# Performance work log

Measured on AMD Instinct MI355X. Metric: run time of the kernel, lower is better.

## Reference

```python
import itertools, math
import jax, jax.numpy as jnp
import numpy as np

N_QUBITS = 8
N_LAYERS = 2
D = 2 ** N_QUBITS
B = 16384
PAIRS = list(itertools.combinations(range(N_QUBITS), 2))
N_PAIRS = len(PAIRS)


def _static():
    s = np.arange(D)
    # ising_masks[p, s] = +1 if bits qi,qj of s differ else -1
    masks = np.stack([
        np.where((((s >> (N_QUBITS - 1 - qi)) & 1) ^ ((s >> (N_QUBITS - 1 - qj)) & 1)).astype(bool), 1.0, -1.0).astype(np.float32)
        for qi, qj in PAIRS])
    # z_signs[k, s] = +1 if bit k of s is 0 else -1
    zsig = np.stack([
        np.where(((s >> (N_QUBITS - 1 - k)) & 1).astype(bool), -1.0, 1.0).astype(np.float32)
        for k in range(N_QUBITS)])
    # CNOT is a permutation: src[i] = i ^ target_mask if ctrl bit of i set, else i
    cidx = np.empty((N_LAYERS, N_QUBITS, D), np.int32)
    for l in range(N_LAYERS):
        rng = l % (N_QUBITS - 1) + 1 if N_QUBITS > 1 else 1
        for ctrl in range(N_QUBITS):
            tgt = (ctrl + rng) % N_QUBITS
            bit = ((s >> (N_QUBITS - 1 - ctrl)) & 1).astype(bool)
            cidx[l, ctrl] = np.where(bit, s ^ (1 << (N_QUBITS - 1 - tgt)), s)
    return jnp.asarray(masks), jnp.asarray(zsig), jnp.asarray(cidx)

ISING_MASKS, Z_SIGNS, CNOT_IDX = _static()


def _ry(a):
    # a: [...] -> [..., 2, 2] complex64
    c, sn = jnp.cos(a * 0.5), jnp.sin(a * 0.5)
    return jnp.stack([jnp.stack([c, -sn], -1), jnp.stack([sn, c], -1)], -2).astype(jnp.complex64)


def _rz(a):
    h = a.astype(jnp.complex64) * 0.5
    z = jnp.zeros_like(h)
    return jnp.stack([jnp.stack([jnp.exp(-1j * h), z], -1), jnp.stack([z, jnp.exp(1j * h)], -1)], -2)


def _rot(w):
    # w: [3] = (phi, theta, omega) -> Rot = RZ(omega) @ RY(theta) @ RZ(phi), shape [2,2]
    return _rz(w[2]) @ _ry(w[1]) @ _rz(w[0])


def _apply_1q(state, gate, k):
    # state: [B, D]; gate: [B,2,2] (batched) or [2,2] (shared)
    Bs, Ds = state.shape
    hi, lo = 1 << k, 1 << (N_QUBITS - k - 1)
    s = state.reshape(Bs, hi, 2, lo)
    if gate.ndim == 3:
        s = jnp.einsum('bij,bhjl->bhil', gate, s)
    else:
        s = jnp.einsum('ij,bhjl->bhil', gate, s)
    return s.reshape(Bs, Ds)


def _forward(theta, phi_enc, j_upper, vqc_weights):
    Bs = theta.shape[0]
    state = jnp.zeros((Bs, D), jnp.complex64).at[:, 0].set(1.0)
    # encoding layer
    for k in range(N_QUBITS):
        state = _apply_1q(state, _ry(theta[:, k]), k)
        state = _apply_1q(state, _rz(phi_enc[:, k]), k)
    # IsingZZ: product over pairs of exp(0.5j*pi*J_p*mask_p) == exp of sum
    exponent = (0.5 * math.pi) * (j_upper @ ISING_MASKS)  # [B, D], real
    state = state * jnp.exp(1j * exponent.astype(jnp.complex64))
    for l in range(N_LAYERS):
        for k in range(N_QUBITS):
            state = _apply_1q(state, _rot(vqc_weights[l, k]), k)
        for k in range(N_QUBITS):
            # CNOT ring as gather permutation (same math as state @ cnot.mT)
            state = jnp.take(state, CNOT_IDX[l, k], axis=1)
        if l < N_LAYERS - 1:
            for k in range(N_QUBITS):
                state = _apply_1q(state, _ry(theta[:, k] * 0.5), k)
                state = _apply_1q(state, _rz(phi_enc[:, k] * 0.5), k)
    probs = jnp.abs(state) ** 2  # [B, D] float32
    return (probs @ Z_SIGNS.T).astype(theta.dtype)  # [B, N_QUBITS]


def setup_inputs() -> dict:
    key = jax.random.key(0)
    k1, k2, k3, k4 = jax.random.split(key, 4)
    return {
        'theta': jax.random.normal(k1, (B, N_QUBITS), jnp.float32),
        'phi_enc': jax.random.normal(k2, (B, N_QUBITS), jnp.float32),
        'j_upper': jax.random.normal(k3, (B, N_PAIRS), jnp.float32),
        'vqc_weights': jax.random.normal(k4, (N_LAYERS, N_QUBITS, 3), jnp.float32),
    }


def reference(theta, phi_enc, j_upper, vqc_weights):
    return _forward(theta, phi_enc, j_upper, vqc_weights)
```

## Files before the change

### kernel.cpp

```cpp
#include <hip/hip_runtime.h>


using f2 = __attribute__((ext_vector_type(2))) float;

__device__ __forceinline__ f2 cmul2(f2 w, f2 z) {
    f2 r;
    r.x = w.x * z.x - w.y * z.y;
    r.y = w.x * z.y + w.y * z.x;
    return r;
}
__device__ __forceinline__ f2 cmadd(f2 acc, f2 w, f2 z) {
    acc.x += w.x * z.x - w.y * z.y;
    acc.y += w.x * z.y + w.y * z.x;
    return acc;
}

__device__ __forceinline__ f2 shflx(f2 v, int m) {
    f2 r; r.x = __shfl_xor(v.x, m, 64); r.y = __shfl_xor(v.y, m, 64); return r;
}

__device__ __forceinline__ float uxor(float f, unsigned u) {
    return __uint_as_float(__float_as_uint(f) ^ u);
}

__device__ __forceinline__ f2 enc_sel(float t, float p, bool hi) {
    float s_, c_, sp_, cp_;
    __sincosf(t * 0.5f, &s_, &c_);
    __sincosf(p * 0.5f, &sp_, &cp_);
    const float m = hi ? s_ : c_;
    f2 r; r.x = m * cp_; r.y = hi ? m * sp_ : -m * sp_;
    return r;
}

template<int VREG, int VLANE, int UREG>
__device__ __forceinline__ void gateU(f2 (&s)[16],
                                      float g00r, float giP, float brP, float g01i)
{
    if constexpr (VLANE == 0) {
        constexpr int pivot = VREG & (-VREG);
        #pragma unroll
        for (int j = 0; j < 16; ++j) {
            if ((j & pivot) != 0) continue;
            const int j2 = j ^ VREG;
            const f2 x = s[j], y = s[j2];
            {
                const bool n = (__builtin_popcount(j & UREG) & 1) != 0;
                const float gi = n ? -giP : giP, br = n ? -brP : brP;
                s[j].x = fmaf(-g01i, y.y, fmaf(br, y.x, fmaf(-gi, x.y, g00r * x.x)));
                s[j].y = fmaf( g01i, y.x, fmaf(br, y.y, fmaf( gi, x.x, g00r * x.y)));
            }
            {
                const bool n = (__builtin_popcount(j2 & UREG) & 1) != 0;
                const float gi = n ? -giP : giP, br = n ? -brP : brP;
                s[j2].x = fmaf(-g01i, x.y, fmaf(br, x.x, fmaf(-gi, y.y, g00r * y.x)));
                s[j2].y = fmaf( g01i, x.x, fmaf(br, x.y, fmaf( gi, y.x, g00r * y.y)));
            }
        }
    } else if constexpr (VREG == 0) {
        #pragma unroll
        for (int j = 0; j < 16; ++j) {
            const f2 w = shflx(s[j], VLANE);
            const f2 x = s[j];
            const bool n = (__builtin_popcount(j & UREG) & 1) != 0;
            const float gi = n ? -giP : giP, br = n ? -brP : brP;
            s[j].x = fmaf(-g01i, w.y, fmaf(br, w.x, fmaf(-gi, x.y, g00r * x.x)));
            s[j].y = fmaf( g01i, w.x, fmaf(br, w.y, fmaf( gi, x.x, g00r * x.y)));
        }
    } else {
        constexpr int pivot = VREG & (-VREG);
        #pragma unroll
        for (int j = 0; j < 16; ++j) {
            if ((j & pivot) != 0) continue;
            const int j2 = j ^ VREG;
            const f2 p1 = shflx(s[j2], VLANE);
            const f2 p2 = shflx(s[j],  VLANE);
            const f2 x = s[j], y = s[j2];
            {
                const bool n = (__builtin_popcount(j & UREG) & 1) != 0;
                const float gi = n ? -giP : giP, br = n ? -brP : brP;
                s[j].x = fmaf(-g01i, p1.y, fmaf(br, p1.x, fmaf(-gi, x.y, g00r * x.x)));
                s[j].y = fmaf( g01i, p1.x, fmaf(br, p1.y, fmaf( gi, x.x, g00r * x.y)));
            }
            {
                const bool n = (__builtin_popcount(j2 & UREG) & 1) != 0;
                const float gi = n ? -giP : giP, br = n ? -brP : brP;
                s[j2].x = fmaf(-g01i, p2.y, fmaf(br, p2.x, fmaf(-gi, y.y, g00r * y.x)));
                s[j2].y = fmaf( g01i, p2.x, fmaf(br, p2.y, fmaf( gi, y.x, g00r * y.y)));
            }
        }
    }
}

#define ROT0(K, VR, VL, UR, SL) do {                                    \
    const float4 g_ = *reinterpret_cast<const float4*>(gates + (K)*4);  \
    gateU<VR, VL, UR>(s, g_.x, uxor(g_.y, SL), uxor(g_.z, SL), g_.w);   \
} while (0)

#define FUSED(K, VR, VL, UR, SL) do {                                   \
    const float4 g_ = *reinterpret_cast<const float4*>(gates + (8+(K))*4); \
    const f2 R00 = {g_.x, g_.y}, R01 = {g_.z, g_.w};                    \
    float c_, s_, cp_, sp_;                                             \
    __sincosf(th[K] * 0.25f, &s_, &c_);                                 \
    __sincosf(ph[K] * 0.25f, &sp_, &cp_);                               \
    const f2 E00 = { c_*cp_, -c_*sp_}, E10 = { s_*cp_,  s_*sp_};        \
    const f2 E01 = {-s_*cp_,  s_*sp_}, E11 = { c_*cp_,  c_*sp_};        \
    const f2 F00 = cmadd(cmul2(R00, E00), R01, E10);                    \
    const f2 F01 = cmadd(cmul2(R00, E01), R01, E11);                    \
    gateU<VR, VL, UR>(s, F00.x, uxor(F00.y, SL), uxor(F01.x, SL), F01.y); \
} while (0)

__global__ __launch_bounds__(64) void prep_gates(const float* __restrict__ w,
                                                 float* __restrict__ g)
{
    const int t = threadIdx.x;
    if (t < 16) {
        const float wph = w[t*3+0], wth = w[t*3+1], wom = w[t*3+2];
        float c_, s_, ca_, sa_, cb_, sb_;
        __sincosf(wth * 0.5f, &s_, &c_);
        __sincosf(0.5f * (wph + wom), &sa_, &ca_);
        __sincosf(0.5f * (wph - wom), &sb_, &cb_);
        float* o = g + t * 4;
        o[0] =  c_*ca_;  o[1] = -c_*sa_;
        o[2] = -s_*cb_;  o[3] = -s_*sb_;
    }
}

__global__ __launch_bounds__(64, 4) void vqc_kernel(
    const float* __restrict__ theta,
    const float* __restrict__ phi,
    const float* __restrict__ jup,
    const float* __restrict__ gates,
    float* __restrict__ out,
    int Btot)
{
    const int wid    = blockIdx.x;
    const int lane   = threadIdx.x & 63;
    const int lane16 = lane & 15;
    const int bq     = wid * 4 + (lane >> 4);
    const int b      = bq < Btot ? bq : Btot - 1;

    float th[8], ph[8];
    {
        const float4* t4 = reinterpret_cast<const float4*>(theta + (size_t)b * 8);
        const float4* p4 = reinterpret_cast<const float4*>(phi   + (size_t)b * 8);
        const float4 a = t4[0], c = t4[1], d = p4[0], e = p4[1];
        th[0]=a.x; th[1]=a.y; th[2]=a.z; th[3]=a.w;
        th[4]=c.x; th[5]=c.y; th[6]=c.z; th[7]=c.w;
        ph[0]=d.x; ph[1]=d.y; ph[2]=d.z; ph[3]=d.w;
        ph[4]=e.x; ph[5]=e.y; ph[6]=e.z; ph[7]=e.w;
    }

    const unsigned s8 = (unsigned)(lane16 & 8) << 28;
    const unsigned s4 = (unsigned)(lane16 & 4) << 29;
    const unsigned s2 = (unsigned)(lane16 & 2) << 30;
    const unsigned s1 = (unsigned)(lane16 & 1) << 31;
    const unsigned sC = s8 ^ s4;
    const unsigned sE = sC ^ s2;
    const unsigned sF = sE ^ s1;

    f2 P = enc_sel(th[4], ph[4], (lane16 & 8) != 0);
    P = cmul2(P, enc_sel(th[5], ph[5], (lane16 & 4) != 0));
    P = cmul2(P, enc_sel(th[6], ph[6], (lane16 & 2) != 0));
    P = cmul2(P, enc_sel(th[7], ph[7], (lane16 & 1) != 0));

    f2 m01[4], m23[4];
    {
        float s0, c0, sp0, cp0, s1_, c1_, sp1, cp1;
        __sincosf(th[0]*0.5f, &s0, &c0); __sincosf(ph[0]*0.5f, &sp0, &cp0);
        __sincosf(th[1]*0.5f, &s1_, &c1_); __sincosf(ph[1]*0.5f, &sp1, &cp1);
        const f2 A0={c0*cp0,-c0*sp0}, A1={s0*cp0,s0*sp0};
        const f2 B0={c1_*cp1,-c1_*sp1}, B1={s1_*cp1,s1_*sp1};
        #pragma unroll
        for (int a = 0; a < 4; ++a)
            m01[a] = cmul2((a & 2) ? A1 : A0, (a & 1) ? B1 : B0);
        __sincosf(th[2]*0.5f, &s0, &c0); __sincosf(ph[2]*0.5f, &sp0, &cp0);
        __sincosf(th[3]*0.5f, &s1_, &c1_); __sincosf(ph[3]*0.5f, &sp1, &cp1);
        const f2 C0={c0*cp0,-c0*sp0}, C1={s0*cp0,s0*sp0};
        const f2 D0={c1_*cp1,-c1_*sp1}, D1={s1_*cp1,s1_*sp1};
        #pragma unroll
        for (int a = 0; a < 4; ++a)
            m23[a] = cmul2((a & 2) ? C1 : C0, (a & 1) ? D1 : D0);
    }

    float c01, c02, c03, c12, c13, c23, Q0, Q1, Q2, Q3, LL;
    {
        const float4* J4 = reinterpret_cast<const float4*>(jup + (size_t)b * 28);
        const float z4 = (lane16 & 8) ? -1.f : 1.f;
        const float z5 = (lane16 & 4) ? -1.f : 1.f;
        const float z6 = (lane16 & 2) ? -1.f : 1.f;
        const float z7 = (lane16 & 1) ? -1.f : 1.f;
        const float4 x0 = J4[0], x1 = J4[1], x2 = J4[2], x3 = J4[3];
        const float4 x4 = J4[4], x5 = J4[5], x6 = J4[6];
        c01 = x0.x; c02 = x0.y; c03 = x0.z;
        Q0  = x0.w*z4 + x1.x*z5 + x1.y*z6 + x1.z*z7;
        c12 = x1.w; c13 = x2.x;
        Q1  = x2.y*z4 + x2.z*z5 + x2.w*z6 + x3.x*z7;
        c23 = x3.y;
        Q2  = x3.z*z4 + x3.w*z5 + x4.x*z6 + x4.y*z7;
        Q3  = x4.z*z4 + x4.w*z5 + x5.x*z6 + x5.y*z7;
        LL  = x5.z*(z4*z5) + x5.w*(z4*z6) + x6.x*(z4*z7)
            + x6.y*(z5*z6) + x6.z*(z5*z7) + x6.w*(z6*z7);
    }

    f2 s[16];
    constexpr float HPI = 1.5707963267948966f;
    #pragma unroll
    for (int j = 0; j < 16; ++j) {
        f2 u = cmul2(cmul2(m01[j >> 2], m23[j & 3]), P);
        float S = LL;
        S += ((__builtin_popcount(j & 0xC) & 1) ? -c01 : c01);
        S += ((__builtin_popcount(j & 0xA) & 1) ? -c02 : c02);
        S += ((__builtin_popcount(j & 0x9) & 1) ? -c03 : c03);
        S += ((__builtin_popcount(j & 0x6) & 1) ? -c12 : c12);
        S += ((__builtin_popcount(j & 0x5) & 1) ? -c13 : c13);
        S += ((__builtin_popcount(j & 0x3) & 1) ? -c23 : c23);
        S += ((j & 8) ? -Q0 : Q0);
        S += ((j & 4) ? -Q1 : Q1);
        S += ((j & 2) ? -Q2 : Q2);
        S += ((j & 1) ? -Q3 : Q3);
        float se, ce;
        __sincosf(-HPI * S, &se, &ce);
        s[j] = cmul2(u, (f2){ce, se});
    }

    ROT0(0, 0x8, 0x0, 0x8, 0u);
    ROT0(1, 0x4, 0x0, 0x4, 0u);
    ROT0(2, 0x2, 0x0, 0x2, 0u);
    ROT0(3, 0x1, 0x0, 0x1, 0u);
    ROT0(4, 0x0, 0x8, 0x0, s8);
    ROT0(5, 0x0, 0x4, 0x0, s4);
    ROT0(6, 0x0, 0x2, 0x0, s2);
    ROT0(7, 0x0, 0x1, 0x0, s1);

    FUSED(0, 0xC, 0x0, 0x7, sF);
    FUSED(1, 0x6, 0x0, 0xC, 0u);
    FUSED(2, 0x3, 0x0, 0xE, 0u);
    FUSED(3, 0x1, 0x8, 0xF, 0u);
    FUSED(4, 0x0, 0xC, 0xF, s8);
    FUSED(5, 0x0, 0x6, 0xF, sC);
    FUSED(6, 0x0, 0x3, 0xF, sE);
    FUSED(7, 0xC, 0x1, 0xF, sF);

    float p[16];
    #pragma unroll
    for (int j = 0; j < 16; ++j) p[j] = fmaf(s[j].y, s[j].y, s[j].x * s[j].x);
    #pragma unroll
    for (int st = 1; st < 16; st <<= 1) {
        #pragma unroll
        for (int j = 0; j < 16; ++j) {
            if ((j & st) != 0) continue;
            const float a = p[j], bb = p[j | st];
            p[j] = a + bb;  p[j | st] = a - bb;
        }
    }
    float o[8];
    o[0] = (__popc(lane16 & 0x6) & 1) ? -p[0xE] : p[0xE];
    o[1] = (__popc(lane16 & 0x3) & 1) ? -p[0xF] : p[0xF];
    o[2] = (__popc(lane16 & 0xF) & 1) ? -p[0x9] : p[0x9];
    o[3] = p[0x3];
    o[4] = (__popc(lane16 & 0x7) & 1) ? -p[0x6] : p[0x6];
    o[5] = (__popc(lane16 & 0xC) & 1) ? -p[0xC] : p[0xC];
    o[6] = (__popc(lane16 & 0x9) & 1) ? -p[0x9] : p[0x9];
    o[7] = (__popc(lane16 & 0x3) & 1) ? -p[0x3] : p[0x3];

    #pragma unroll
    for (int m = 1; m <= 8; m <<= 1) {
        #pragma unroll
        for (int q = 0; q < 8; ++q) o[q] += __shfl_xor(o[q], m, 64);
    }

    if (lane16 == 0 && bq < Btot) {
        float4* op = reinterpret_cast<float4*>(out + (size_t)bq * 8);
        op[0] = make_float4(o[0], o[1], o[2], o[3]);
        op[1] = make_float4(o[4], o[5], o[6], o[7]);
    }
}

extern "C" void kernel_launch(void* const* d_in, const int* in_sizes, int n_in,
                              void* d_out, int out_size, void* d_ws, size_t ws_size,
                              hipStream_t stream) {
    const float* theta = (const float*)d_in[0];
    const float* phi   = (const float*)d_in[1];
    const float* jup   = (const float*)d_in[2];
    const float* w     = (const float*)d_in[3];
    float* out   = (float*)d_out;
    float* gates = (float*)d_ws;

    const int B = in_sizes[0] / 8;
    hipLaunchKernelGGL(prep_gates, dim3(1), dim3(64), 0, stream, w, gates);

    const int blocks = (B + 3) / 4;
    hipLaunchKernelGGL(vqc_kernel, dim3(blocks), dim3(64), 0, stream,
                       theta, phi, jup, gates, out, B);
}
```

Measured before the change: 82.54 us.

## Spread each sample over 32 lanes and fold gate prep into main kernel

Each 256-qubit state is now split across 32 lanes holding 8 amplitudes each, instead of 16 lanes holding 16, so the per-thread register footprint shrinks and more lanes work on each sample. The separate prep_gates launch is removed. Each lane now computes the rotation gate matrices itself and shares them through readlane, and the fused encoding-rotation gates are precomputed per lane and broadcast with shuffles. The trade-off is more cross-lane shuffles per gate, one extra reduction stage, and redundant trig work in every wave.

```diff
diff --git a/kernel.cpp b/kernel.cpp
--- a/kernel.cpp
+++ b/kernel.cpp
@@ -33,13 +33,13 @@
 }
 
 template<int VREG, int VLANE, int UREG>
-__device__ __forceinline__ void gateU(f2 (&s)[16],
-                                      float g00r, float giP, float brP, float g01i)
+__device__ __forceinline__ void gateU8(f2 (&s)[8],
+                                       float g00r, float giP, float brP, float g01i)
 {
     if constexpr (VLANE == 0) {
         constexpr int pivot = VREG & (-VREG);
         #pragma unroll
-        for (int j = 0; j < 16; ++j) {
+        for (int j = 0; j < 8; ++j) {
             if ((j & pivot) != 0) continue;
             const int j2 = j ^ VREG;
             const f2 x = s[j], y = s[j2];
@@ -58,7 +58,7 @@
         }
     } else if constexpr (VREG == 0) {
         #pragma unroll
-        for (int j = 0; j < 16; ++j) {
+        for (int j = 0; j < 8; ++j) {
             const f2 w = shflx(s[j], VLANE);
             const f2 x = s[j];
             const bool n = (__builtin_popcount(j & UREG) & 1) != 0;
@@ -69,7 +69,7 @@
     } else {
         constexpr int pivot = VREG & (-VREG);
         #pragma unroll
-        for (int j = 0; j < 16; ++j) {
+        for (int j = 0; j < 8; ++j) {
             if ((j & pivot) != 0) continue;
             const int j2 = j ^ VREG;
             const f2 p1 = shflx(s[j2], VLANE);
@@ -91,53 +91,45 @@
     }
 }
 
-#define ROT0(K, VR, VL, UR, SL) do {                                    \
-    const float4 g_ = *reinterpret_cast<const float4*>(gates + (K)*4);  \
-    gateU<VR, VL, UR>(s, g_.x, uxor(g_.y, SL), uxor(g_.z, SL), g_.w);   \
+#define RL(x, t) __int_as_float(__builtin_amdgcn_readlane(__float_as_int(x), (t)))
+
+#define ROT0(K, VR, VL, UR, SL) do {                                       \
+    const float g0r = RL(q00r, K), g0i = RL(q00i, K);                      \
+    const float g1r = RL(q01r, K), g1i = RL(q01i, K);                      \
+    gateU8<VR, VL, UR>(s, g0r, uxor(g0i, SL), uxor(g1r, SL), g1i);         \
 } while (0)
 
-#define FUSED(K, VR, VL, UR, SL) do {                                   \
-    const float4 g_ = *reinterpret_cast<const float4*>(gates + (8+(K))*4); \
-    const f2 R00 = {g_.x, g_.y}, R01 = {g_.z, g_.w};                    \
-    float c_, s_, cp_, sp_;                                             \
-    __sincosf(th[K] * 0.25f, &s_, &c_);                                 \
-    __sincosf(ph[K] * 0.25f, &sp_, &cp_);                               \
-    const f2 E00 = { c_*cp_, -c_*sp_}, E10 = { s_*cp_,  s_*sp_};        \
-    const f2 E01 = {-s_*cp_,  s_*sp_}, E11 = { c_*cp_,  c_*sp_};        \
-    const f2 F00 = cmadd(cmul2(R00, E00), R01, E10);                    \
-    const f2 F01 = cmadd(cmul2(R00, E01), R01, E11);                    \
-    gateU<VR, VL, UR>(s, F00.x, uxor(F00.y, SL), uxor(F01.x, SL), F01.y); \
+#define FUSED(K, VR, VL, UR, SL) do {                                      \
+    const float f0r = __shfl(F00x, K, 8), f0i = __shfl(F00y, K, 8);        \
+    const float f1r = __shfl(F01x, K, 8), f1i = __shfl(F01y, K, 8);        \
+    gateU8<VR, VL, UR>(s, f0r, uxor(f0i, SL), uxor(f1r, SL), f1i);         \
 } while (0)
 
-__global__ __launch_bounds__(64) void prep_gates(const float* __restrict__ w,
-                                                 float* __restrict__ g)
-{
-    const int t = threadIdx.x;
-    if (t < 16) {
-        const float wph = w[t*3+0], wth = w[t*3+1], wom = w[t*3+2];
-        float c_, s_, ca_, sa_, cb_, sb_;
-        __sincosf(wth * 0.5f, &s_, &c_);
-        __sincosf(0.5f * (wph + wom), &sa_, &ca_);
-        __sincosf(0.5f * (wph - wom), &sb_, &cb_);
-        float* o = g + t * 4;
-        o[0] =  c_*ca_;  o[1] = -c_*sa_;
-        o[2] = -s_*cb_;  o[3] = -s_*sb_;
-    }
-}
-
-__global__ __launch_bounds__(64, 4) void vqc_kernel(
+__global__ __launch_bounds__(256, 7) void vqc_kernel(
     const float* __restrict__ theta,
     const float* __restrict__ phi,
     const float* __restrict__ jup,
-    const float* __restrict__ gates,
+    const float* __restrict__ w,
     float* __restrict__ out,
     int Btot)
 {
-    const int wid    = blockIdx.x;
-    const int lane   = threadIdx.x & 63;
-    const int lane16 = lane & 15;
-    const int bq     = wid * 4 + (lane >> 4);
-    const int b      = bq < Btot ? bq : Btot - 1;
+    const int gtid  = blockIdx.x * 256 + threadIdx.x;
+    const int lane  = threadIdx.x & 63;
+    const int lane5 = lane & 31;
+    const int bq    = gtid >> 5;
+    const int b     = bq < Btot ? bq : Btot - 1;
+
+    float q00r, q00i, q01r, q01i;
+    {
+        const int gt = lane & 15;
+        const float wph = w[gt*3+0], wth = w[gt*3+1], wom = w[gt*3+2];
+        float gc_, gs_, ca_, sa_, cb_, sb_;
+        __sincosf(wth * 0.5f, &gs_, &gc_);
+        __sincosf(0.5f * (wph + wom), &sa_, &ca_);
+        __sincosf(0.5f * (wph - wom), &sb_, &cb_);
+        q00r =  gc_*ca_;  q00i = -gc_*sa_;
+        q01r = -gs_*cb_;  q01i = -gs_*sb_;
+    }
 
     float th[8], ph[8];
     {
@@ -150,126 +142,137 @@
         ph[4]=e.x; ph[5]=e.y; ph[6]=e.z; ph[7]=e.w;
     }
 
-    const unsigned s8 = (unsigned)(lane16 & 8) << 28;
-    const unsigned s4 = (unsigned)(lane16 & 4) << 29;
-    const unsigned s2 = (unsigned)(lane16 & 2) << 30;
-    const unsigned s1 = (unsigned)(lane16 & 1) << 31;
-    const unsigned sC = s8 ^ s4;
-    const unsigned sE = sC ^ s2;
-    const unsigned sF = sE ^ s1;
-
-    f2 P = enc_sel(th[4], ph[4], (lane16 & 8) != 0);
-    P = cmul2(P, enc_sel(th[5], ph[5], (lane16 & 4) != 0));
-    P = cmul2(P, enc_sel(th[6], ph[6], (lane16 & 2) != 0));
-    P = cmul2(P, enc_sel(th[7], ph[7], (lane16 & 1) != 0));
-
-    f2 m01[4], m23[4];
-    {
-        float s0, c0, sp0, cp0, s1_, c1_, sp1, cp1;
+    float F00x, F00y, F01x, F01y;
+    {
+        const int Kq = lane5 & 7;
+        const float thK = theta[(size_t)b * 8 + Kq];
+        const float phK = phi  [(size_t)b * 8 + Kq];
+        float c_, s_, cp_, sp_;
+        __sincosf(thK * 0.25f, &s_, &c_);
+        __sincosf(phK * 0.25f, &sp_, &cp_);
+        const f2 R00 = { __shfl(q00r, 8 + Kq, 16), __shfl(q00i, 8 + Kq, 16) };
+        const f2 R01 = { __shfl(q01r, 8 + Kq, 16), __shfl(q01i, 8 + Kq, 16) };
+        const f2 E00 = { c_*cp_, -c_*sp_}, E10 = { s_*cp_,  s_*sp_};
+        const f2 E01 = {-s_*cp_,  s_*sp_}, E11 = { c_*cp_,  c_*sp_};
+        const f2 F00 = cmadd(cmul2(R00, E00), R01, E10);
+        const f2 F01 = cmadd(cmul2(R00, E01), R01, E11);
+        F00x = F00.x; F00y = F00.y; F01x = F01.x; F01y = F01.y;
+    }
+
+    const unsigned t16 = (unsigned)(lane5 & 16) << 27;
+    const unsigned t8  = (unsigned)(lane5 & 8)  << 28;
+    const unsigned t4  = (unsigned)(lane5 & 4)  << 29;
+    const unsigned t2  = (unsigned)(lane5 & 2)  << 30;
+    const unsigned t1  = (unsigned)(lane5 & 1)  << 31;
+    const unsigned s18 = t16 ^ t8;
+    const unsigned s1C = s18 ^ t4;
+    const unsigned s1E = s1C ^ t2;
+    const unsigned s1F = s1E ^ t1;
+
+    f2 P = enc_sel(th[3], ph[3], (lane5 & 16) != 0);
+    P = cmul2(P, enc_sel(th[4], ph[4], (lane5 & 8) != 0));
+    P = cmul2(P, enc_sel(th[5], ph[5], (lane5 & 4) != 0));
+    P = cmul2(P, enc_sel(th[6], ph[6], (lane5 & 2) != 0));
+    P = cmul2(P, enc_sel(th[7], ph[7], (lane5 & 1) != 0));
+
+    f2 m012[8];
+    {
+        float s0, c0, sp0, cp0;
         __sincosf(th[0]*0.5f, &s0, &c0); __sincosf(ph[0]*0.5f, &sp0, &cp0);
-        __sincosf(th[1]*0.5f, &s1_, &c1_); __sincosf(ph[1]*0.5f, &sp1, &cp1);
         const f2 A0={c0*cp0,-c0*sp0}, A1={s0*cp0,s0*sp0};
-        const f2 B0={c1_*cp1,-c1_*sp1}, B1={s1_*cp1,s1_*sp1};
-        #pragma unroll
-        for (int a = 0; a < 4; ++a)
-            m01[a] = cmul2((a & 2) ? A1 : A0, (a & 1) ? B1 : B0);
+        __sincosf(th[1]*0.5f, &s0, &c0); __sincosf(ph[1]*0.5f, &sp0, &cp0);
+        const f2 B0={c0*cp0,-c0*sp0}, B1={s0*cp0,s0*sp0};
         __sincosf(th[2]*0.5f, &s0, &c0); __sincosf(ph[2]*0.5f, &sp0, &cp0);
-        __sincosf(th[3]*0.5f, &s1_, &c1_); __sincosf(ph[3]*0.5f, &sp1, &cp1);
         const f2 C0={c0*cp0,-c0*sp0}, C1={s0*cp0,s0*sp0};
-        const f2 D0={c1_*cp1,-c1_*sp1}, D1={s1_*cp1,s1_*sp1};
-        #pragma unroll
-        for (int a = 0; a < 4; ++a)
-            m23[a] = cmul2((a & 2) ? C1 : C0, (a & 1) ? D1 : D0);
-    }
-
-    float c01, c02, c03, c12, c13, c23, Q0, Q1, Q2, Q3, LL;
+        #pragma unroll
+        for (int a = 0; a < 8; ++a)
+            m012[a] = cmul2(cmul2((a & 4) ? A1 : A0, (a & 2) ? B1 : B0),
+                            (a & 1) ? C1 : C0);
+    }
+
+    float c01, c02, c12, Q0, Q1, Q2, LL;
     {
         const float4* J4 = reinterpret_cast<const float4*>(jup + (size_t)b * 28);
-        const float z4 = (lane16 & 8) ? -1.f : 1.f;
-        const float z5 = (lane16 & 4) ? -1.f : 1.f;
-        const float z6 = (lane16 & 2) ? -1.f : 1.f;
-        const float z7 = (lane16 & 1) ? -1.f : 1.f;
+        const float z3 = (lane5 & 16) ? -1.f : 1.f;
+        const float z4 = (lane5 & 8)  ? -1.f : 1.f;
+        const float z5 = (lane5 & 4)  ? -1.f : 1.f;
+        const float z6 = (lane5 & 2)  ? -1.f : 1.f;
+        const float z7 = (lane5 & 1)  ? -1.f : 1.f;
         const float4 x0 = J4[0], x1 = J4[1], x2 = J4[2], x3 = J4[3];
         const float4 x4 = J4[4], x5 = J4[5], x6 = J4[6];
-        c01 = x0.x; c02 = x0.y; c03 = x0.z;
-        Q0  = x0.w*z4 + x1.x*z5 + x1.y*z6 + x1.z*z7;
-        c12 = x1.w; c13 = x2.x;
-        Q1  = x2.y*z4 + x2.z*z5 + x2.w*z6 + x3.x*z7;
-        c23 = x3.y;
-        Q2  = x3.z*z4 + x3.w*z5 + x4.x*z6 + x4.y*z7;
-        Q3  = x4.z*z4 + x4.w*z5 + x5.x*z6 + x5.y*z7;
-        LL  = x5.z*(z4*z5) + x5.w*(z4*z6) + x6.x*(z4*z7)
+        c01 = x0.x; c02 = x0.y; c12 = x1.w;
+        Q0  = x0.z*z3 + x0.w*z4 + x1.x*z5 + x1.y*z6 + x1.z*z7;
+        Q1  = x2.x*z3 + x2.y*z4 + x2.z*z5 + x2.w*z6 + x3.x*z7;
+        Q2  = x3.y*z3 + x3.z*z4 + x3.w*z5 + x4.x*z6 + x4.y*z7;
+        LL  = x4.z*(z3*z4) + x4.w*(z3*z5) + x5.x*(z3*z6) + x5.y*(z3*z7)
+            + x5.z*(z4*z5) + x5.w*(z4*z6) + x6.x*(z4*z7)
             + x6.y*(z5*z6) + x6.z*(z5*z7) + x6.w*(z6*z7);
     }
 
-    f2 s[16];
+    f2 s[8];
     constexpr float HPI = 1.5707963267948966f;
     #pragma unroll
-    for (int j = 0; j < 16; ++j) {
-        f2 u = cmul2(cmul2(m01[j >> 2], m23[j & 3]), P);
+    for (int j = 0; j < 8; ++j) {
+        f2 u = cmul2(m012[j], P);
         float S = LL;
-        S += ((__builtin_popcount(j & 0xC) & 1) ? -c01 : c01);
-        S += ((__builtin_popcount(j & 0xA) & 1) ? -c02 : c02);
-        S += ((__builtin_popcount(j & 0x9) & 1) ? -c03 : c03);
-        S += ((__builtin_popcount(j & 0x6) & 1) ? -c12 : c12);
-        S += ((__builtin_popcount(j & 0x5) & 1) ? -c13 : c13);
-        S += ((__builtin_popcount(j & 0x3) & 1) ? -c23 : c23);
-        S += ((j & 8) ? -Q0 : Q0);
-        S += ((j & 4) ? -Q1 : Q1);
-        S += ((j & 2) ? -Q2 : Q2);
-        S += ((j & 1) ? -Q3 : Q3);
+        S += ((__builtin_popcount(j & 6) & 1) ? -c01 : c01);
+        S += ((__builtin_popcount(j & 5) & 1) ? -c02 : c02);
+        S += ((__builtin_popcount(j & 3) & 1) ? -c12 : c12);
+        S += ((j & 4) ? -Q0 : Q0);
+        S += ((j & 2) ? -Q1 : Q1);
+        S += ((j & 1) ? -Q2 : Q2);
         float se, ce;
         __sincosf(-HPI * S, &se, &ce);
         s[j] = cmul2(u, (f2){ce, se});
     }
 
-    ROT0(0, 0x8, 0x0, 0x8, 0u);
-    ROT0(1, 0x4, 0x0, 0x4, 0u);
-    ROT0(2, 0x2, 0x0, 0x2, 0u);
-    ROT0(3, 0x1, 0x0, 0x1, 0u);
-    ROT0(4, 0x0, 0x8, 0x0, s8);
-    ROT0(5, 0x0, 0x4, 0x0, s4);
-    ROT0(6, 0x0, 0x2, 0x0, s2);
-    ROT0(7, 0x0, 0x1, 0x0, s1);
-
-    FUSED(0, 0xC, 0x0, 0x7, sF);
-    FUSED(1, 0x6, 0x0, 0xC, 0u);
-    FUSED(2, 0x3, 0x0, 0xE, 0u);
-    FUSED(3, 0x1, 0x8, 0xF, 0u);
-    FUSED(4, 0x0, 0xC, 0xF, s8);
-    FUSED(5, 0x0, 0x6, 0xF, sC);
-    FUSED(6, 0x0, 0x3, 0xF, sE);
-    FUSED(7, 0xC, 0x1, 0xF, sF);
-
-    float p[16];
-    #pragma unroll
-    for (int j = 0; j < 16; ++j) p[j] = fmaf(s[j].y, s[j].y, s[j].x * s[j].x);
-    #pragma unroll
-    for (int st = 1; st < 16; st <<= 1) {
-        #pragma unroll
-        for (int j = 0; j < 16; ++j) {
+    ROT0(0, 0x4, 0x00, 0x4, 0u);
+    ROT0(1, 0x2, 0x00, 0x2, 0u);
+    ROT0(2, 0x1, 0x00, 0x1, 0u);
+    ROT0(3, 0x0, 0x10, 0x0, t16);
+    ROT0(4, 0x0, 0x08, 0x0, t8);
+    ROT0(5, 0x0, 0x04, 0x0, t4);
+    ROT0(6, 0x0, 0x02, 0x0, t2);
+    ROT0(7, 0x0, 0x01, 0x0, t1);
+
+    FUSED(0, 0x6, 0x00, 0x3, s1F);
+    FUSED(1, 0x3, 0x00, 0x6, 0u);
+    FUSED(2, 0x1, 0x10, 0x7, 0u);
+    FUSED(3, 0x0, 0x18, 0x7, t16);
+    FUSED(4, 0x0, 0x0C, 0x7, s18);
+    FUSED(5, 0x0, 0x06, 0x7, s1C);
+    FUSED(6, 0x0, 0x03, 0x7, s1E);
+    FUSED(7, 0x6, 0x01, 0x7, s1F);
+
+    float p[8];
+    #pragma unroll
+    for (int j = 0; j < 8; ++j) p[j] = fmaf(s[j].y, s[j].y, s[j].x * s[j].x);
+    #pragma unroll
+    for (int st = 1; st < 8; st <<= 1) {
+        #pragma unroll
+        for (int j = 0; j < 8; ++j) {
             if ((j & st) != 0) continue;
             const float a = p[j], bb = p[j | st];
             p[j] = a + bb;  p[j | st] = a - bb;
         }
     }
     float o[8];
-    o[0] = (__popc(lane16 & 0x6) & 1) ? -p[0xE] : p[0xE];
-    o[1] = (__popc(lane16 & 0x3) & 1) ? -p[0xF] : p[0xF];
-    o[2] = (__popc(lane16 & 0xF) & 1) ? -p[0x9] : p[0x9];
-    o[3] = p[0x3];
-    o[4] = (__popc(lane16 & 0x7) & 1) ? -p[0x6] : p[0x6];
-    o[5] = (__popc(lane16 & 0xC) & 1) ? -p[0xC] : p[0xC];
-    o[6] = (__popc(lane16 & 0x9) & 1) ? -p[0x9] : p[0x9];
-    o[7] = (__popc(lane16 & 0x3) & 1) ? -p[0x3] : p[0x3];
-
-    #pragma unroll
-    for (int m = 1; m <= 8; m <<= 1) {
+    o[0] = (__popc(lane5 & 0x06) & 1) ? -p[7] : p[7];
+    o[1] = (__popc(lane5 & 0x13) & 1) ? -p[7] : p[7];
+    o[2] = (__popc(lane5 & 0x1F) & 1) ? -p[4] : p[4];
+    o[3] = (__popc(lane5 & 0x10) & 1) ? -p[1] : p[1];
+    o[4] = (__popc(lane5 & 0x07) & 1) ? -p[3] : p[3];
+    o[5] = (__popc(lane5 & 0x0C) & 1) ? -p[6] : p[6];
+    o[6] = (__popc(lane5 & 0x19) & 1) ? -p[4] : p[4];
+    o[7] = (__popc(lane5 & 0x13) & 1) ? -p[1] : p[1];
+
+    #pragma unroll
+    for (int m = 1; m <= 16; m <<= 1) {
         #pragma unroll
         for (int q = 0; q < 8; ++q) o[q] += __shfl_xor(o[q], m, 64);
     }
 
-    if (lane16 == 0 && bq < Btot) {
+    if (lane5 == 0 && bq < Btot) {
         float4* op = reinterpret_cast<float4*>(out + (size_t)bq * 8);
         op[0] = make_float4(o[0], o[1], o[2], o[3]);
         op[1] = make_float4(o[4], o[5], o[6], o[7]);
@@ -283,13 +286,10 @@
     const float* phi   = (const float*)d_in[1];
     const float* jup   = (const float*)d_in[2];
     const float* w     = (const float*)d_in[3];
-    float* out   = (float*)d_out;
-    float* gates = (float*)d_ws;
+    float* out = (float*)d_out;
 
     const int B = in_sizes[0] / 8;
-    hipLaunchKernelGGL(prep_gates, dim3(1), dim3(64), 0, stream, w, gates);
-
-    const int blocks = (B + 3) / 4;
-    hipLaunchKernelGGL(vqc_kernel, dim3(blocks), dim3(64), 0, stream,
-                       theta, phi, jup, gates, out, B);
-}
+    const int blocks = (B + 7) / 8;
+    hipLaunchKernelGGL(vqc_kernel, dim3(blocks), dim3(256), 0, stream,
+                       theta, phi, jup, w, out, B);
+}
```

New measurement: 84.11 us. Within noise of the previous version (+1.9%).

## Replace shuffles with DPP/swizzle and fold gate prep into main kernel

Applied to the files above, without the earlier changes.

Cross-lane exchanges in the gate application and the final reduction now use DPP row operations and ds_swizzle instead of generic __shfl_xor, which is meant to avoid the LDS-backed bpermute path. The separate prep_gates launch is removed. Each lane computes one rotation gate and broadcasts it with readlane, and the fused encoding×rotation gates are computed once per lane and broadcast with swizzle, so the per-gate sincos work and the global gate loads go away. Blocks grow from 64 to 256 threads. The added risks are the correctness of the DPP/swizzle patterns and some extra register pressure.

```diff
diff --git a/kernel.cpp b/kernel.cpp
--- a/kernel.cpp
+++ b/kernel.cpp
@@ -15,13 +15,34 @@
     return acc;
 }
 
-__device__ __forceinline__ f2 shflx(f2 v, int m) {
-    f2 r; r.x = __shfl_xor(v.x, m, 64); r.y = __shfl_xor(v.y, m, 64); return r;
-}
-
 __device__ __forceinline__ float uxor(float f, unsigned u) {
     return __uint_as_float(__float_as_uint(f) ^ u);
 }
+
+template<int M>
+__device__ __forceinline__ float xlane(float v) {
+    const int x = __float_as_int(v);
+    int r;
+    if constexpr (M == 1)
+        r = __builtin_amdgcn_update_dpp(x, x, 0xB1, 0xF, 0xF, false);
+    else if constexpr (M == 2)
+        r = __builtin_amdgcn_update_dpp(x, x, 0x4E, 0xF, 0xF, false);
+    else if constexpr (M == 3)
+        r = __builtin_amdgcn_update_dpp(x, x, 0x1B, 0xF, 0xF, false);
+    else if constexpr (M == 8)
+        r = __builtin_amdgcn_update_dpp(x, x, 0x128, 0xF, 0xF, false);
+    else
+        r = __builtin_amdgcn_ds_swizzle(x, (M << 10) | 0x1F);
+    return __int_as_float(r);
+}
+template<int M>
+__device__ __forceinline__ f2 xshfl2(f2 v) {
+    f2 r; r.x = xlane<M>(v.x); r.y = xlane<M>(v.y); return r;
+}
+
+#define BC8(x, K) __int_as_float(__builtin_amdgcn_ds_swizzle( \
+    __float_as_int(x), ((K) << 5) | 0x18))
+#define SW117(x) __int_as_float(__builtin_amdgcn_ds_swizzle(__float_as_int(x), 0x117))
 
 __device__ __forceinline__ f2 enc_sel(float t, float p, bool hi) {
     float s_, c_, sp_, cp_;
@@ -59,7 +80,7 @@
     } else if constexpr (VREG == 0) {
         #pragma unroll
         for (int j = 0; j < 16; ++j) {
-            const f2 w = shflx(s[j], VLANE);
+            const f2 w = xshfl2<VLANE>(s[j]);
             const f2 x = s[j];
             const bool n = (__builtin_popcount(j & UREG) & 1) != 0;
             const float gi = n ? -giP : giP, br = n ? -brP : brP;
@@ -72,8 +93,8 @@
         for (int j = 0; j < 16; ++j) {
             if ((j & pivot) != 0) continue;
             const int j2 = j ^ VREG;
-            const f2 p1 = shflx(s[j2], VLANE);
-            const f2 p2 = shflx(s[j],  VLANE);
+            const f2 p1 = xshfl2<VLANE>(s[j2]);
+            const f2 p2 = xshfl2<VLANE>(s[j]);
             const f2 x = s[j], y = s[j2];
             {
                 const bool n = (__builtin_popcount(j & UREG) & 1) != 0;
@@ -91,53 +112,49 @@
     }
 }
 
-#define ROT0(K, VR, VL, UR, SL) do {                                    \
-    const float4 g_ = *reinterpret_cast<const float4*>(gates + (K)*4);  \
-    gateU<VR, VL, UR>(s, g_.x, uxor(g_.y, SL), uxor(g_.z, SL), g_.w);   \
+#define RL(x, t) __int_as_float(__builtin_amdgcn_readlane(__float_as_int(x), (t)))
+
+#define ROT0(K, VR, VL, UR, SL) do {                                       \
+    const float g0r = RL(q00r, K), g0i = RL(q00i, K);                      \
+    const float g1r = RL(q01r, K), g1i = RL(q01i, K);                      \
+    gateU<VR, VL, UR>(s, g0r, uxor(g0i, SL), uxor(g1r, SL), g1i);          \
 } while (0)
 
-#define FUSED(K, VR, VL, UR, SL) do {                                   \
-    const float4 g_ = *reinterpret_cast<const float4*>(gates + (8+(K))*4); \
-    const f2 R00 = {g_.x, g_.y}, R01 = {g_.z, g_.w};                    \
-    float c_, s_, cp_, sp_;                                             \
-    __sincosf(th[K] * 0.25f, &s_, &c_);                                 \
-    __sincosf(ph[K] * 0.25f, &sp_, &cp_);                               \
-    const f2 E00 = { c_*cp_, -c_*sp_}, E10 = { s_*cp_,  s_*sp_};        \
-    const f2 E01 = {-s_*cp_,  s_*sp_}, E11 = { c_*cp_,  c_*sp_};        \
-    const f2 F00 = cmadd(cmul2(R00, E00), R01, E10);                    \
-    const f2 F01 = cmadd(cmul2(R00, E01), R01, E11);                    \
-    gateU<VR, VL, UR>(s, F00.x, uxor(F00.y, SL), uxor(F01.x, SL), F01.y); \
+#define FUSED(K, VR, VL, UR, SL) do {                                      \
+    const float f0r = BC8(F00x, K), f0i = BC8(F00y, K);                    \
+    const float f1r = BC8(F01x, K), f1i = BC8(F01y, K);                    \
+    gateU<VR, VL, UR>(s, f0r, uxor(f0i, SL), uxor(f1r, SL), f1i);          \
 } while (0)
 
-__global__ __launch_bounds__(64) void prep_gates(const float* __restrict__ w,
-                                                 float* __restrict__ g)
-{
-    const int t = threadIdx.x;
-    if (t < 16) {
-        const float wph = w[t*3+0], wth = w[t*3+1], wom = w[t*3+2];
-        float c_, s_, ca_, sa_, cb_, sb_;
-        __sincosf(wth * 0.5f, &s_, &c_);
-        __sincosf(0.5f * (wph + wom), &sa_, &ca_);
-        __sincosf(0.5f * (wph - wom), &sb_, &cb_);
-        float* o = g + t * 4;
-        o[0] =  c_*ca_;  o[1] = -c_*sa_;
-        o[2] = -s_*cb_;  o[3] = -s_*sb_;
-    }
-}
-
-__global__ __launch_bounds__(64, 4) void vqc_kernel(
+__global__ __launch_bounds__(256, 4) void vqc_kernel(
     const float* __restrict__ theta,
     const float* __restrict__ phi,
     const float* __restrict__ jup,
-    const float* __restrict__ gates,
+    const float* __restrict__ w,
     float* __restrict__ out,
     int Btot)
 {
-    const int wid    = blockIdx.x;
+    const int gtid   = blockIdx.x * 256 + threadIdx.x;
     const int lane   = threadIdx.x & 63;
     const int lane16 = lane & 15;
-    const int bq     = wid * 4 + (lane >> 4);
+    const int bq     = gtid >> 4;
     const int b      = bq < Btot ? bq : Btot - 1;
+
+    float q00r, q00i, q01r, q01i;
+    {
+        const int gt = lane & 15;
+        const float wph = w[gt*3+0], wth = w[gt*3+1], wom = w[gt*3+2];
+        float gc_, gs_, ca_, sa_, cb_, sb_;
+        __sincosf(wth * 0.5f, &gs_, &gc_);
+        __sincosf(0.5f * (wph + wom), &sa_, &ca_);
+        __sincosf(0.5f * (wph - wom), &sb_, &cb_);
+        q00r =  gc_*ca_;  q00i = -gc_*sa_;
+        q01r = -gs_*cb_;  q01i = -gs_*sb_;
+    }
+
+    const int Kq = lane & 7;
+    const float thK = theta[(size_t)b * 8 + Kq];
+    const float phK = phi  [(size_t)b * 8 + Kq];
 
     float th[8], ph[8];
     {
@@ -148,6 +165,20 @@
         th[4]=c.x; th[5]=c.y; th[6]=c.z; th[7]=c.w;
         ph[0]=d.x; ph[1]=d.y; ph[2]=d.z; ph[3]=d.w;
         ph[4]=e.x; ph[5]=e.y; ph[6]=e.z; ph[7]=e.w;
+    }
+
+    float F00x, F00y, F01x, F01y;
+    {
+        float c_, s_, cp_, sp_;
+        __sincosf(thK * 0.25f, &s_, &c_);
+        __sincosf(phK * 0.25f, &sp_, &cp_);
+        const f2 R00 = { SW117(q00r), SW117(q00i) };
+        const f2 R01 = { SW117(q01r), SW117(q01i) };
+        const f2 E00 = { c_*cp_, -c_*sp_}, E10 = { s_*cp_,  s_*sp_};
+        const f2 E01 = {-s_*cp_,  s_*sp_}, E11 = { c_*cp_,  c_*sp_};
+        const f2 F00 = cmadd(cmul2(R00, E00), R01, E10);
+        const f2 F01 = cmadd(cmul2(R00, E01), R01, E11);
+        F00x = F00.x; F00y = F00.y; F01x = F01.x; F01y = F01.y;
     }
 
     const unsigned s8 = (unsigned)(lane16 & 8) << 28;
@@ -264,10 +295,13 @@
     o[7] = (__popc(lane16 & 0x3) & 1) ? -p[0x3] : p[0x3];
 
     #pragma unroll
-    for (int m = 1; m <= 8; m <<= 1) {
-        #pragma unroll
-        for (int q = 0; q < 8; ++q) o[q] += __shfl_xor(o[q], m, 64);
-    }
+    for (int q = 0; q < 8; ++q) o[q] += xlane<1>(o[q]);
+    #pragma unroll
+    for (int q = 0; q < 8; ++q) o[q] += xlane<2>(o[q]);
+    #pragma unroll
+    for (int q = 0; q < 8; ++q) o[q] += xlane<4>(o[q]);
+    #pragma unroll
+    for (int q = 0; q < 8; ++q) o[q] += xlane<8>(o[q]);
 
     if (lane16 == 0 && bq < Btot) {
         float4* op = reinterpret_cast<float4*>(out + (size_t)bq * 8);
@@ -283,13 +317,10 @@
     const float* phi   = (const float*)d_in[1];
     const float* jup   = (const float*)d_in[2];
     const float* w     = (const float*)d_in[3];
-    float* out   = (float*)d_out;
-    float* gates = (float*)d_ws;
+    float* out = (float*)d_out;
 
     const int B = in_sizes[0] / 8;
-    hipLaunchKernelGGL(prep_gates, dim3(1), dim3(64), 0, stream, w, gates);
-
-    const int blocks = (B + 3) / 4;
-    hipLaunchKernelGGL(vqc_kernel, dim3(blocks), dim3(64), 0, stream,
-                       theta, phi, jup, gates, out, B);
-}
+    const int blocks = (B * 16 + 255) / 256;
+    hipLaunchKernelGGL(vqc_kernel, dim3(blocks), dim3(256), 0, stream,
+                       theta, phi, jup, w, out, B);
+}
```

Result: faster. 78.78 us (-4.6%).
